# Optimization experiments

Hardware: AMD Instinct MI355X
Metric: run time of the kernel (lower is better)

## Reference

```python
import jax, jax.numpy as jnp
import numpy as np

HEADS = 4
DIM_HEAD = 32
DIM = 128
HIDDEN = HEADS * DIM_HEAD  # 128
LN_EPS = 1e-6


def setup_inputs() -> dict:
    key = jax.random.key(0)
    ks = jax.random.split(key, 4)
    b, X, Y, Z = 4, 32, 32, 32
    x = jax.random.normal(ks[0], (b, X, Y, Z, DIM), dtype=jnp.float32)
    # 1x1x1 convs are pointwise linears: kernel [in, out]
    w_qkv = jax.random.normal(ks[1], (DIM, 3 * HIDDEN), dtype=jnp.float32) * (DIM ** -0.5)
    w_out = jax.random.normal(ks[2], (HIDDEN, DIM), dtype=jnp.float32) * (HIDDEN ** -0.5)
    b_out = jax.random.normal(ks[3], (DIM,), dtype=jnp.float32) * 0.02
    ln_scale = jnp.ones((DIM,), dtype=jnp.float32)
    ln_bias = jnp.zeros((DIM,), dtype=jnp.float32)
    return {"x": x, "w_qkv": w_qkv, "w_out": w_out, "b_out": b_out,
            "ln_scale": ln_scale, "ln_bias": ln_bias}


def reference(x, w_qkv, w_out, b_out, ln_scale, ln_bias):
    b, X, Y, Z, c = x.shape
    n = X * Y * Z
    scale = DIM_HEAD ** (-0.5)

    # 1x1x1 conv (no bias) == pointwise matmul over channels
    qkv = jnp.einsum('bxyzc,cd->bxyzd', x, w_qkv)  # [b,X,Y,Z,3*hidden]
    q, k, v = jnp.split(qkv, 3, axis=-1)

    # rearrange 'b x y z (h c) -> b h c n'
    def to_bhcn(t):
        return t.reshape(b, n, HEADS, DIM_HEAD).transpose(0, 2, 3, 1)

    q, k, v = to_bhcn(q), to_bhcn(k), to_bhcn(v)

    q = jax.nn.softmax(q, axis=-2) * scale   # softmax over feature dim d
    k = jax.nn.softmax(k, axis=-1)           # softmax over token dim n

    context = jnp.einsum('bhdn,bhcn->bhdc', k, v)   # [b,h,d,c] small d=c=32
    out = jnp.einsum('bhde,bhdn->bhen', context, q) # [b,h,e,n]

    # rearrange 'b h c n -> b x y z (h c)' (cubic volume, matching original)
    out = out.transpose(0, 3, 1, 2).reshape(b, X, Y, Z, HIDDEN)

    # final 1x1x1 conv with bias
    out = jnp.einsum('bxyzh,hc->bxyzc', out, w_out) + b_out

    # LayerNorm over last axis (flax default eps=1e-6, with scale+bias)
    mu = jnp.mean(out, axis=-1, keepdims=True)
    var = jnp.mean(jnp.square(out - mu), axis=-1, keepdims=True)
    out = (out - mu) * jax.lax.rsqrt(var + LN_EPS) * ln_scale + ln_bias
    return out
```

## Files before the change

kernel.cpp:

```cpp
#include <hip/hip_runtime.h>
#include <hip/hip_bf16.h>

typedef _Float16 f16;
typedef _Float16 f16x4 __attribute__((ext_vector_type(4)));
typedef _Float16 f16x8 __attribute__((ext_vector_type(8)));
typedef float f32x4 __attribute__((ext_vector_type(4)));

#define MFMA(a, b, c) __builtin_amdgcn_mfma_f32_16x16x32_f16((a), (b), (c), 0, 0, 0)

#define BB 4
#define NPOS 32768
#define HH 4
#define NBLK 1024
#define STATB 2304
#define LDP 136
#define LDQ 40

__device__ __forceinline__ f16x8 ldx8(const float* p) {
  float4 a = *(const float4*)p;
  float4 b = *(const float4*)(p + 4);
  return (f16x8){(f16)a.x, (f16)a.y, (f16)a.z, (f16)a.w,
                 (f16)b.x, (f16)b.y, (f16)b.z, (f16)b.w};
}

__global__ __launch_bounds__(256)
void la_k0_prep(const float* __restrict__ wqkv, const float* __restrict__ wout,
                f16* __restrict__ wkvF, f16* __restrict__ wqF,
                f16* __restrict__ woutT) {
  const int g0 = blockIdx.x * 256 + threadIdx.x;
  for (int i = g0; i < 32768; i += 16384) {
    int j = i & 7, l = (i >> 3) & 63, ks = (i >> 9) & 3, nt = (i >> 11) & 3,
        h = i >> 13;
    int n = 16 * nt + (l & 15);
    int c = 32 * ks + 8 * (l >> 4) + j;
    int col = (n < 32) ? (128 + h * 32 + n) : (256 + h * 32 + (n - 32));
    wkvF[i] = (f16)wqkv[c * 384 + col];
  }
  {
    int i = g0;
    int j = i & 7, l = (i >> 3) & 63, ks = (i >> 9) & 3, a = (i >> 11) & 1,
        h = i >> 12;
    int n = 16 * a + (l & 15);
    int c = 32 * ks + 8 * (l >> 4) + j;
    wqF[i] = (f16)wqkv[c * 384 + h * 32 + n];
  }
  if (g0 < 128 * 128) {
    int k = g0 & 127, n = g0 >> 7;
    woutT[g0] = (f16)wout[k * 128 + n];
  }
}

__global__ __launch_bounds__(256, 4)
void la_k1_stats(const float* __restrict__ x, const f16* __restrict__ wkvF,
                 char* __restrict__ stats) {
  const int blk = blockIdx.x, t = threadIdx.x;
  const int w = t >> 6, l = t & 63, lg = l >> 4, ln = l & 15;

  __shared__ __align__(16) f16 EV[2][64 * LDP];

  const float* xb = x + (size_t)blk * (128 * 128);
  f16x8 xf[2][4];
#pragma unroll
  for (int mi = 0; mi < 2; ++mi)
#pragma unroll
    for (int ks = 0; ks < 4; ++ks)
      xf[mi][ks] = ldx8(xb + (32 * w + 16 * mi + ln) * 128 + 32 * ks + 8 * lg);

  const f32x4 Z4 = {0.f, 0.f, 0.f, 0.f};

  auto logits = [&](int h, f32x4 (&acc)[2][4]) {
#pragma unroll
    for (int mi = 0; mi < 2; ++mi)
#pragma unroll
      for (int nt = 0; nt < 4; ++nt) acc[mi][nt] = Z4;
#pragma unroll
    for (int ks = 0; ks < 4; ++ks) {
#pragma unroll
      for (int nt = 0; nt < 4; ++nt) {
        f16x8 bf = *(const f16x8*)(wkvF + (((h * 4 + nt) * 4 + ks) << 9) + l * 8);
        acc[0][nt] = MFMA(xf[0][ks], bf, acc[0][nt]);
        acc[1][nt] = MFMA(xf[1][ks], bf, acc[1][nt]);
      }
    }
  };

  auto phaseA = [&](int h, f32x4 (&acc)[2][4]) {
    f16* E = (f16*)EV[h & 1];
    float sl[2] = {0.f, 0.f};
#pragma unroll
    for (int nt = 0; nt < 2; ++nt)
#pragma unroll
      for (int mi = 0; mi < 2; ++mi) {
        float e0 = __expf(acc[mi][nt][0]);
        float e1 = __expf(acc[mi][nt][1]);
        float e2 = __expf(acc[mi][nt][2]);
        float e3 = __expf(acc[mi][nt][3]);
        sl[nt] += (e0 + e1) + (e2 + e3);
        *(f16x4*)&E[(16 * nt + ln) * LDP + 32 * w + 16 * mi + 4 * lg] =
            (f16x4){(f16)e0, (f16)e1, (f16)e2, (f16)e3};
        f32x4 vv = acc[mi][nt + 2];
        *(f16x4*)&E[(32 + 16 * nt + ln) * LDP + 32 * w + 16 * mi + 4 * lg] =
            (f16x4){(f16)vv[0], (f16)vv[1], (f16)vv[2], (f16)vv[3]};
      }
#pragma unroll
    for (int nt = 0; nt < 2; ++nt) {
      sl[nt] += __shfl_xor(sl[nt], 16);
      sl[nt] += __shfl_xor(sl[nt], 32);
    }
    f16* sp = (f16*)(stats + (size_t)(blk * HH + h) * STATB + 2048);
    if (lg == 0) {
      sp[ln * 4 + w] = (f16)sl[0];
      sp[(16 + ln) * 4 + w] = (f16)sl[1];
    }
  };

  auto phaseB = [&](int h) {
    __syncthreads();
    const f16* E = (const f16*)EV[h & 1];
    const int tm = w >> 1, tn = w & 1;
    f32x4 tacc = Z4;
#pragma unroll
    for (int ks = 0; ks < 4; ++ks) {
      f16x8 ea = *(const f16x8*)&E[(16 * tm + ln) * LDP + 32 * ks + 8 * lg];
      f16x8 vb = *(const f16x8*)&E[(32 + 16 * tn + ln) * LDP + 32 * ks + 8 * lg];
      tacc = MFMA(ea, vb, tacc);
    }
    f16* tp = (f16*)(stats + (size_t)(blk * HH + h) * STATB);
#pragma unroll
    for (int r = 0; r < 4; ++r)
      tp[(16 * tm + 4 * lg + r) * 32 + 16 * tn + ln] = (f16)tacc[r];
  };

  f32x4 accA[2][4], accB[2][4];
  logits(0, accA);
  phaseA(0, accA); logits(1, accB); phaseB(0);
  phaseA(1, accB); logits(2, accA); phaseB(1);
  phaseA(2, accA); logits(3, accB); phaseB(2);
  phaseA(3, accB); phaseB(3);
}

__global__ __launch_bounds__(256)
void la_k2_combine(const char* __restrict__ stats, f16* __restrict__ ctxN) {
  const int gid = blockIdx.x;
  const int bh = gid >> 5, d = gid & 31;
  const int b = bh >> 2, h = bh & 3;
  const int t = threadIdx.x, w = t >> 6, l = t & 63;
  const int c = t & 31, grp = t >> 5;
  __shared__ float redt[4][32];
  __shared__ float reds[4];

  float sg = 0.f, tc = 0.f;
  for (int i = grp; i < 256; i += 8) {
    const char* ub = stats + (size_t)((b * 256 + i) * HH + h) * STATB;
    tc += (float)((const f16*)ub)[d * 32 + c];
    f16x4 s4 = *(const f16x4*)(ub + 2048 + d * 8);
    sg += ((float)s4[0] + (float)s4[1]) + ((float)s4[2] + (float)s4[3]);
  }
  tc += __shfl_xor(tc, 32);
  sg += __shfl_xor(sg, 32);
  if (l < 32) redt[w][l] = tc;
  if (l == 0) reds[w] = sg;
  __syncthreads();
  if (t < 32) {
    float tt = (redt[0][t] + redt[1][t]) + (redt[2][t] + redt[3][t]);
    float ss = (reds[0] + reds[1]) + (reds[2] + reds[3]);
    ctxN[((size_t)bh * 32 + d) * 32 + t] = (f16)(tt / ss);
  }
}

__global__ __launch_bounds__(256)
void la_k2b_fold(const f16* __restrict__ ctxN, const f16* __restrict__ woutT,
                 f16* __restrict__ GT) {
  const int b = blockIdx.x, t = threadIdx.x;
  const int h = t >> 6, l = t & 63, lg = l >> 4, ln = l & 15;
  const f32x4 Z4 = {0.f, 0.f, 0.f, 0.f};

  const f16* cb = ctxN + (size_t)((b * HH + h) * 32) * 32;
  f16x8 bfrag[2];
#pragma unroll
  for (int nt = 0; nt < 2; ++nt)
    bfrag[nt] = *(const f16x8*)(cb + (16 * nt + ln) * 32 + 8 * lg);

  f16* gb = GT + (size_t)b * (128 * 128);
#pragma unroll
  for (int mt = 0; mt < 8; ++mt) {
    f16x8 af = *(const f16x8*)(woutT + (16 * mt + ln) * 128 + 32 * h + 8 * lg);
#pragma unroll
    for (int nt = 0; nt < 2; ++nt) {
      f32x4 acc = MFMA(af, bfrag[nt], Z4);
#pragma unroll
      for (int r = 0; r < 4; ++r)
        gb[(size_t)(16 * mt + 4 * lg + r) * 128 + 32 * h + 16 * nt + ln] =
            (f16)acc[r];
    }
  }
}

__global__ __launch_bounds__(256, 3)
void la_k3_out(const float* __restrict__ x, const f16* __restrict__ wqF,
               const f16* __restrict__ GT, const float* __restrict__ bout,
               const float* __restrict__ lns, const float* __restrict__ lnb,
               float* __restrict__ out) {
  const int blk = blockIdx.x, t = threadIdx.x;
  const int w = t >> 6, l = t & 63, lg = l >> 4, ln = l & 15;
  const int b = blk >> 8;

  __shared__ __align__(16) f16 GTs[16384];
  __shared__ __align__(16) f16 Qs[128 * LDQ];

  {
    const f16* gbm = GT + (size_t)b * (128 * 128);
#pragma unroll
    for (int i = 0; i < 8; ++i) {
      int idx = i * 256 + t;
      int row = idx >> 4;
      int col8 = idx & 15;
      f16x8 v = *(const f16x8*)(gbm + row * 128 + col8 * 8);
      int chunk = (col8 >> 2) * 8 + (row >> 4);
      int slot = (col8 & 3) * 16 + (row & 15);
      *(f16x8*)&GTs[(chunk << 9) + slot * 8] = v;
    }
  }

  const float* xb = x + (size_t)blk * (128 * 128);
  f16x8 xf[2][4];
#pragma unroll
  for (int nt = 0; nt < 2; ++nt)
#pragma unroll
    for (int ks = 0; ks < 4; ++ks)
      xf[nt][ks] = ldx8(xb + (32 * w + 16 * nt + ln) * 128 + 32 * ks + 8 * lg);

  const f32x4 Z4 = {0.f, 0.f, 0.f, 0.f};

  f32x4 y[2][8];
#pragma unroll
  for (int mi = 0; mi < 2; ++mi)
#pragma unroll
    for (int nt = 0; nt < 8; ++nt) y[mi][nt] = Z4;

  auto qlog = [&](int h, f32x4 (&qa)[2][2]) {
#pragma unroll
    for (int mt = 0; mt < 2; ++mt)
#pragma unroll
      for (int nt = 0; nt < 2; ++nt) qa[mt][nt] = Z4;
#pragma unroll
    for (int ks = 0; ks < 4; ++ks) {
      f16x8 a0 = *(const f16x8*)(wqF + (((h * 2 + 0) * 4 + ks) << 9) + l * 8);
      f16x8 a1 = *(const f16x8*)(wqF + (((h * 2 + 1) * 4 + ks) << 9) + l * 8);
#pragma unroll
      for (int nt = 0; nt < 2; ++nt) {
        qa[0][nt] = MFMA(a0, xf[nt][ks], qa[0][nt]);
        qa[1][nt] = MFMA(a1, xf[nt][ks], qa[1][nt]);
      }
    }
  };

  auto consume = [&](int h, f32x4 (&qa)[2][2]) {
#pragma unroll
    for (int nt = 0; nt < 2; ++nt) {
      float s = 0.f;
#pragma unroll
      for (int mt = 0; mt < 2; ++mt)
#pragma unroll
        for (int r = 0; r < 4; ++r) {
          qa[mt][nt][r] = __expf(qa[mt][nt][r]);
          s += qa[mt][nt][r];
        }
      s += __shfl_xor(s, 16);
      s += __shfl_xor(s, 32);
      const float inv = 0.17677669529663688f / s;
#pragma unroll
      for (int mt = 0; mt < 2; ++mt) {
        *(f16x4*)&Qs[(32 * w + 16 * nt + ln) * LDQ + 16 * mt + 4 * lg] =
            (f16x4){(f16)(qa[mt][nt][0] * inv), (f16)(qa[mt][nt][1] * inv),
                    (f16)(qa[mt][nt][2] * inv), (f16)(qa[mt][nt][3] * inv)};
      }
    }
  };

  auto ymfma = [&](int h) {
#pragma unroll
    for (int mi = 0; mi < 2; ++mi) {
      f16x8 af = *(const f16x8*)&Qs[(32 * w + 16 * mi + ln) * LDQ + 8 * lg];
#pragma unroll
      for (int nt = 0; nt < 8; ++nt) {
        f16x8 bf = *(const f16x8*)&GTs[((h * 8 + nt) << 9) + l * 8];
        y[mi][nt] = MFMA(af, bf, y[mi][nt]);
      }
    }
  };

  f32x4 qaA[2][2], qaB[2][2];
  qlog(0, qaA);
  consume(0, qaA);
  qlog(1, qaB);
  __syncthreads();
  ymfma(0);
  consume(1, qaB); qlog(2, qaA); ymfma(1);
  consume(2, qaA); qlog(3, qaB); ymfma(2);
  consume(3, qaB); ymfma(3);

  float bv[8], sv[8], b2[8];
#pragma unroll
  for (int nt = 0; nt < 8; ++nt) {
    int col = 16 * nt + ln;
    bv[nt] = bout[col];
    sv[nt] = lns[col];
    b2[nt] = lnb[col];
  }
#pragma unroll
  for (int mi = 0; mi < 2; ++mi)
#pragma unroll
    for (int r = 0; r < 4; ++r) {
      float sum = 0.f;
#pragma unroll
      for (int nt = 0; nt < 8; ++nt) {
        y[mi][nt][r] += bv[nt];
        sum += y[mi][nt][r];
      }
      sum += __shfl_xor(sum, 1);
      sum += __shfl_xor(sum, 2);
      sum += __shfl_xor(sum, 4);
      sum += __shfl_xor(sum, 8);
      const float mean = sum * (1.f / 128.f);
      float var = 0.f;
#pragma unroll
      for (int nt = 0; nt < 8; ++nt) {
        float dv = y[mi][nt][r] - mean;
        var = fmaf(dv, dv, var);
      }
      var += __shfl_xor(var, 1);
      var += __shfl_xor(var, 2);
      var += __shfl_xor(var, 4);
      var += __shfl_xor(var, 8);
      const float inv = rsqrtf(var * (1.f / 128.f) + 1e-6f);
      const int pos = blk * 128 + 32 * w + 16 * mi + 4 * lg + r;
      float* op = out + (size_t)pos * 128;
#pragma unroll
      for (int nt = 0; nt < 8; ++nt)
        op[16 * nt + ln] = (y[mi][nt][r] - mean) * inv * sv[nt] + b2[nt];
    }
}

extern "C" void kernel_launch(void* const* d_in, const int* in_sizes, int n_in,
                              void* d_out, int out_size, void* d_ws, size_t ws_size,
                              hipStream_t stream) {
  const float* x = (const float*)d_in[0];
  const float* w_qkv = (const float*)d_in[1];
  const float* w_out = (const float*)d_in[2];
  const float* b_out = (const float*)d_in[3];
  const float* ln_s = (const float*)d_in[4];
  const float* ln_b = (const float*)d_in[5];
  float* out = (float*)d_out;

  char* ws = (char*)d_ws;
  char* stats = ws;
  f16* wkvF = (f16*)(ws + 9437184);
  f16* wqF = (f16*)(ws + 9437184 + 65536);
  f16* woutT = (f16*)(ws + 9437184 + 65536 + 32768);
  f16* ctxN = (f16*)(ws + 9437184 + 65536 + 32768 + 32768);
  f16* GT = (f16*)ws;

  la_k0_prep<<<dim3(64), 256, 0, stream>>>(w_qkv, w_out, wkvF, wqF, woutT);
  la_k1_stats<<<dim3(NBLK), 256, 0, stream>>>(x, wkvF, stats);
  la_k2_combine<<<dim3(512), 256, 0, stream>>>(stats, ctxN);
  la_k2b_fold<<<dim3(BB), 256, 0, stream>>>(ctxN, woutT, GT);
  la_k3_out<<<dim3(NBLK), 256, 0, stream>>>(x, wqF, GT, b_out, ln_s, ln_b, out);
}
```

Measured before the change: 86.68 us.

## Keep softmaxed Q in registers and read fragment-ordered G directly from global

The fold kernel now writes the combined context-times-W_out matrix already in MFMA B-fragment order, and the Q weight rows are permuted so that the Q logits' accumulator layout matches the A-operand layout of the output MFMA. The output kernel can then build A fragments directly in registers, dropping both shared-memory buffers, the staging copy and the block barrier. Occupancy is raised from 3 to 4 blocks per CU. The trade-off is that G fragments are now read from global/L2 by every wave instead of from LDS.

```diff
diff --git a/kernel.cpp b/kernel.cpp
--- a/kernel.cpp
+++ b/kernel.cpp
@@ -14,7 +14,6 @@
 #define NBLK 1024
 #define STATB 2304
 #define LDP 136
-#define LDQ 40
 
 __device__ __forceinline__ f16x8 ldx8(const float* p) {
   float4 a = *(const float4*)p;
@@ -40,7 +39,8 @@
     int i = g0;
     int j = i & 7, l = (i >> 3) & 63, ks = (i >> 9) & 3, a = (i >> 11) & 1,
         h = i >> 12;
-    int n = 16 * a + (l & 15);
+    int row = l & 15;
+    int n = 8 * (row >> 2) + 4 * a + (row & 3);
     int c = 32 * ks + 8 * (l >> 4) + j;
     wqF[i] = (f16)wqkv[c * 384 + h * 32 + n];
   }
@@ -170,7 +170,7 @@
 
 __global__ __launch_bounds__(256)
 void la_k2b_fold(const f16* __restrict__ ctxN, const f16* __restrict__ woutT,
-                 f16* __restrict__ GT) {
+                 f16* __restrict__ GTF) {
   const int b = blockIdx.x, t = threadIdx.x;
   const int h = t >> 6, l = t & 63, lg = l >> 4, ln = l & 15;
   const f32x4 Z4 = {0.f, 0.f, 0.f, 0.f};
@@ -181,7 +181,7 @@
   for (int nt = 0; nt < 2; ++nt)
     bfrag[nt] = *(const f16x8*)(cb + (16 * nt + ln) * 32 + 8 * lg);
 
-  f16* gb = GT + (size_t)b * (128 * 128);
+  f16* gf = GTF + (size_t)b * 16384;
 #pragma unroll
   for (int mt = 0; mt < 8; ++mt) {
     f16x8 af = *(const f16x8*)(woutT + (16 * mt + ln) * 128 + 32 * h + 8 * lg);
@@ -189,39 +189,24 @@
     for (int nt = 0; nt < 2; ++nt) {
       f32x4 acc = MFMA(af, bfrag[nt], Z4);
 #pragma unroll
-      for (int r = 0; r < 4; ++r)
-        gb[(size_t)(16 * mt + 4 * lg + r) * 128 + 32 * h + 16 * nt + ln] =
+      for (int r = 0; r < 4; ++r) {
+        int dsub = 16 * nt + ln;
+        gf[((h * 8 + mt) << 9) + (16 * (dsub >> 3) + 4 * lg + r) * 8 + (dsub & 7)] =
             (f16)acc[r];
-    }
-  }
-}
-
-__global__ __launch_bounds__(256, 3)
+      }
+    }
+  }
+}
+
+__global__ __launch_bounds__(256, 4)
 void la_k3_out(const float* __restrict__ x, const f16* __restrict__ wqF,
-               const f16* __restrict__ GT, const float* __restrict__ bout,
+               const f16* __restrict__ GTF, const float* __restrict__ bout,
                const float* __restrict__ lns, const float* __restrict__ lnb,
                float* __restrict__ out) {
   const int blk = blockIdx.x, t = threadIdx.x;
   const int w = t >> 6, l = t & 63, lg = l >> 4, ln = l & 15;
   const int b = blk >> 8;
 
-  __shared__ __align__(16) f16 GTs[16384];
-  __shared__ __align__(16) f16 Qs[128 * LDQ];
-
-  {
-    const f16* gbm = GT + (size_t)b * (128 * 128);
-#pragma unroll
-    for (int i = 0; i < 8; ++i) {
-      int idx = i * 256 + t;
-      int row = idx >> 4;
-      int col8 = idx & 15;
-      f16x8 v = *(const f16x8*)(gbm + row * 128 + col8 * 8);
-      int chunk = (col8 >> 2) * 8 + (row >> 4);
-      int slot = (col8 & 3) * 16 + (row & 15);
-      *(f16x8*)&GTs[(chunk << 9) + slot * 8] = v;
-    }
-  }
-
   const float* xb = x + (size_t)blk * (128 * 128);
   f16x8 xf[2][4];
 #pragma unroll
@@ -231,6 +216,7 @@
       xf[nt][ks] = ldx8(xb + (32 * w + 16 * nt + ln) * 128 + 32 * ks + 8 * lg);
 
   const f32x4 Z4 = {0.f, 0.f, 0.f, 0.f};
+  const f16* gf = GTF + (size_t)b * 16384;
 
   f32x4 y[2][8];
 #pragma unroll
@@ -255,7 +241,7 @@
     }
   };
 
-  auto consume = [&](int h, f32x4 (&qa)[2][2]) {
+  auto consume = [&](f32x4 (&qa)[2][2], f16x8 (&af)[2]) {
 #pragma unroll
     for (int nt = 0; nt < 2; ++nt) {
       float s = 0.f;
@@ -269,36 +255,29 @@
       s += __shfl_xor(s, 16);
       s += __shfl_xor(s, 32);
       const float inv = 0.17677669529663688f / s;
-#pragma unroll
-      for (int mt = 0; mt < 2; ++mt) {
-        *(f16x4*)&Qs[(32 * w + 16 * nt + ln) * LDQ + 16 * mt + 4 * lg] =
-            (f16x4){(f16)(qa[mt][nt][0] * inv), (f16)(qa[mt][nt][1] * inv),
-                    (f16)(qa[mt][nt][2] * inv), (f16)(qa[mt][nt][3] * inv)};
-      }
-    }
-  };
-
-  auto ymfma = [&](int h) {
-#pragma unroll
-    for (int mi = 0; mi < 2; ++mi) {
-      f16x8 af = *(const f16x8*)&Qs[(32 * w + 16 * mi + ln) * LDQ + 8 * lg];
-#pragma unroll
-      for (int nt = 0; nt < 8; ++nt) {
-        f16x8 bf = *(const f16x8*)&GTs[((h * 8 + nt) << 9) + l * 8];
-        y[mi][nt] = MFMA(af, bf, y[mi][nt]);
-      }
+      af[nt] = (f16x8){(f16)(qa[0][nt][0] * inv), (f16)(qa[0][nt][1] * inv),
+                       (f16)(qa[0][nt][2] * inv), (f16)(qa[0][nt][3] * inv),
+                       (f16)(qa[1][nt][0] * inv), (f16)(qa[1][nt][1] * inv),
+                       (f16)(qa[1][nt][2] * inv), (f16)(qa[1][nt][3] * inv)};
+    }
+  };
+
+  auto ymfma = [&](int h, f16x8 (&af)[2]) {
+#pragma unroll
+    for (int nc = 0; nc < 8; ++nc) {
+      f16x8 bf = *(const f16x8*)(gf + (((h * 8 + nc) << 9) + l * 8));
+      y[0][nc] = MFMA(af[0], bf, y[0][nc]);
+      y[1][nc] = MFMA(af[1], bf, y[1][nc]);
     }
   };
 
   f32x4 qaA[2][2], qaB[2][2];
-  qlog(0, qaA);
-  consume(0, qaA);
-  qlog(1, qaB);
-  __syncthreads();
-  ymfma(0);
-  consume(1, qaB); qlog(2, qaA); ymfma(1);
-  consume(2, qaA); qlog(3, qaB); ymfma(2);
-  consume(3, qaB); ymfma(3);
+  f16x8 afA[2], afB[2];
+  qlog(0, qaA); qlog(1, qaB);
+  consume(qaA, afA); ymfma(0, afA); qlog(2, qaA);
+  consume(qaB, afB); ymfma(1, afB); qlog(3, qaB);
+  consume(qaA, afA); ymfma(2, afA);
+  consume(qaB, afB); ymfma(3, afB);
 
   float bv[8], sv[8], b2[8];
 #pragma unroll
@@ -359,11 +338,11 @@
   f16* wqF = (f16*)(ws + 9437184 + 65536);
   f16* woutT = (f16*)(ws + 9437184 + 65536 + 32768);
   f16* ctxN = (f16*)(ws + 9437184 + 65536 + 32768 + 32768);
-  f16* GT = (f16*)ws;
+  f16* GTF = (f16*)ws;
 
   la_k0_prep<<<dim3(64), 256, 0, stream>>>(w_qkv, w_out, wkvF, wqF, woutT);
   la_k1_stats<<<dim3(NBLK), 256, 0, stream>>>(x, wkvF, stats);
   la_k2_combine<<<dim3(512), 256, 0, stream>>>(stats, ctxN);
-  la_k2b_fold<<<dim3(BB), 256, 0, stream>>>(ctxN, woutT, GT);
-  la_k3_out<<<dim3(NBLK), 256, 0, stream>>>(x, wqF, GT, b_out, ln_s, ln_b, out);
-}
+  la_k2b_fold<<<dim3(BB), 256, 0, stream>>>(ctxN, woutT, GTF);
+  la_k3_out<<<dim3(NBLK), 256, 0, stream>>>(x, wqF, GTF, b_out, ln_s, ln_b, out);
+}
```

Result: no change. 85.61 us (-1.2%).
